# Performance work log

Hardware: AMD Instinct MI355X
Metric: run time of the kernel (lower is better)

Reference implementation:

```python
import jax, jax.numpy as jnp
import numpy as np

B, C, W, H = 2, 64, 96, 96  # N = W*H = 9216 spatial positions


def conv1x1(x, w, b):
    # x: (B, Cin, W, H), w: (Cout, Cin), b: (Cout,) -> (B, Cout, W, H)
    return jnp.einsum('bchw,oc->bohw', x, w) + b[None, :, None, None]


def setup_inputs() -> dict:
    key = jax.random.key(0)
    ks = jax.random.split(key, 4)
    c8 = C // 8
    s = 0.05  # small weight scale keeps softmax logits in a sane range
    return {
        'x': jax.random.normal(ks[0], (B, C, W, H), jnp.float32),
        'wq': jax.random.normal(ks[1], (c8, C), jnp.float32) * s,
        'bq': jnp.zeros((c8,), jnp.float32),
        'wk': jax.random.normal(ks[2], (c8, C), jnp.float32) * s,
        'bk': jnp.zeros((c8,), jnp.float32),
        'wv': jax.random.normal(ks[3], (C, C), jnp.float32) * s,
        'bv': jnp.zeros((C,), jnp.float32),
        'gamma': jnp.full((1,), 0.5, jnp.float32),
    }


def reference(x, wq, bq, wk, bk, wv, bv, gamma):
    b, c, w, h = x.shape
    n = w * h
    q = conv1x1(x, wq, bq).reshape(b, -1, n)   # (B, C//8, N)
    k = conv1x1(x, wk, bk).reshape(b, -1, n)   # (B, C//8, N)
    v = conv1x1(x, wv, bv).reshape(b, c, n)    # (B, C, N)
    energy = jnp.einsum('bci,bcj->bij', q, k)  # (B, N, N)
    attn = jax.nn.softmax(energy, axis=-1)
    # torch.bmm(v, attn): out[b,c,i] = sum_j v[b,c,j] * attn[b,j,i]
    out = jnp.einsum('bcj,bji->bci', v, attn).reshape(b, c, w, h)
    return gamma * out + x
```

## Files before the change

kernel.cpp:

```cpp
#include <hip/hip_runtime.h>

using half2v  = __attribute__((ext_vector_type(2))) _Float16;
using half4   = __attribute__((ext_vector_type(4))) _Float16;
using half8   = __attribute__((ext_vector_type(8))) _Float16;
using floatx4 = __attribute__((ext_vector_type(4))) float;

constexpr int BATCH = 2;
constexpr int NPOS  = 96 * 96;
constexpr int NT    = NPOS / 16;
constexpr int NST   = NPOS / 32;

#define EXP2(x) __builtin_amdgcn_exp2f(x)
#define MFMA16(A, B, C) __builtin_amdgcn_mfma_f32_16x16x16f16(A, B, C, 0, 0, 0)
#define MFMA32(A, B, C) __builtin_amdgcn_mfma_f32_16x16x32_f16(A, B, C, 0, 0, 0)

__device__ inline half8 p8_of(floatx4 e0, floatx4 e1) {
    half2v a0 = __builtin_bit_cast(half2v,
        __builtin_amdgcn_cvt_pkrtz(EXP2(e0[0]), EXP2(e0[1])));
    half2v a1 = __builtin_bit_cast(half2v,
        __builtin_amdgcn_cvt_pkrtz(EXP2(e0[2]), EXP2(e0[3])));
    half2v a2 = __builtin_bit_cast(half2v,
        __builtin_amdgcn_cvt_pkrtz(EXP2(e1[0]), EXP2(e1[1])));
    half2v a3 = __builtin_bit_cast(half2v,
        __builtin_amdgcn_cvt_pkrtz(EXP2(e1[2]), EXP2(e1[3])));
    half8 p = {a0[0], a0[1], a1[0], a1[1], a2[0], a2[1], a3[0], a3[1]};
    return p;
}

__global__ __launch_bounds__(256) void qkv_kernel(
    const float* __restrict__ x,
    const float* __restrict__ wq, const float* __restrict__ bq,
    const float* __restrict__ wk, const float* __restrict__ bk,
    const float* __restrict__ wv, const float* __restrict__ bv,
    _Float16* __restrict__ Qf, _Float16* __restrict__ Kf,
    _Float16* __restrict__ Vf)
{
    __shared__ float W[80][64];
    __shared__ float bias[80];
    __shared__ float qs[32][9];
    __shared__ float ks[32][9];
    __shared__ _Float16 vs[32][72];
    const int tid = threadIdx.x;
    for (int idx = tid; idx < 80 * 64; idx += 256) {
        int o = idx >> 6, c = idx & 63;
        float w;
        if (o < 8)       w = wq[o * 64 + c];
        else if (o < 16) w = wk[(o - 8) * 64 + c];
        else             w = wv[(o - 16) * 64 + c];
        W[o][c] = w;
    }
    if (tid < 80) {
        float bb;
        if (tid < 8)       bb = bq[tid];
        else if (tid < 16) bb = bk[tid - 8];
        else               bb = bv[tid - 16];
        bias[tid] = bb;
    }
    __syncthreads();

    const int js = blockIdx.x;
    const int b  = blockIdx.y;
    const int part = tid >> 5;
    const int jl   = tid & 31;
    const int i    = js * 32 + jl;

    float xr[64];
    #pragma unroll
    for (int c = 0; c < 64; ++c)
        xr[c] = x[(size_t)(b * 64 + c) * NPOS + i];

    #pragma unroll
    for (int q = 0; q < 10; ++q) {
        const int o = part * 10 + q;
        float s = bias[o];
        #pragma unroll
        for (int c4 = 0; c4 < 16; ++c4) {
            float4 w4 = *(const float4*)&W[o][c4 * 4];
            s += w4.x * xr[c4*4+0] + w4.y * xr[c4*4+1]
               + w4.z * xr[c4*4+2] + w4.w * xr[c4*4+3];
        }
        if (o < 8)       qs[jl][o] = s;
        else if (o < 16) ks[jl][o - 8] = s;
        else             vs[jl][o - 16] = (_Float16)s;
    }
    __syncthreads();

    const size_t tile = (size_t)b * NST + js;
    {
        const int ct = tid >> 6, l = tid & 63;
        const int g = l >> 4, cl = l & 15;
        half8 o8;
        #pragma unroll
        for (int idx = 0; idx < 8; ++idx)
            o8[idx] = vs[8 * g + idx][16 * ct + cl];
        *(half8*)&Vf[(tile * 256 + ct * 64 + l) * 8] = o8;
    }
    if (tid < 128) {
        const int l = tid >> 1, e = tid & 1;
        const int m = l & 15, g = l >> 4;
        const int jsrc = 8 * (m >> 2) + 4 * e + (m & 3);
        constexpr float LOG2E = 1.44269504088896f;
        half4 qh;
        #pragma unroll
        for (int r = 0; r < 4; ++r)
            qh[r] = (g < 2) ? (_Float16)(qs[jsrc][4 * g + r] * LOG2E)
                            : (_Float16)0.f;
        ((half4*)Qf)[(tile * 64 + l) * 2 + e] = qh;
    } else {
        const int t = tid - 128;
        const int ht = t >> 6, l = t & 63;
        const int il = l & 15, g = l >> 4;
        const int it = js * 2 + ht;
        half4 kh;
        #pragma unroll
        for (int r = 0; r < 4; ++r) {
            if (g < 2)       kh[r] = (_Float16)ks[16 * ht + il][4 * g + r];
            else if (g == 2) kh[r] = (r < 2) ? (_Float16)1.f : (_Float16)0.f;
            else             kh[r] = (_Float16)0.f;
        }
        ((half4*)Kf)[(size_t)(b * NT + it) * 64 + l] = kh;
    }
}

template<int JSPLIT>
__global__ __launch_bounds__(256, 3) void attn_kernel(
    const _Float16* __restrict__ Qf, const _Float16* __restrict__ Kf,
    const _Float16* __restrict__ Vf,
    float* __restrict__ part, float* __restrict__ part_rs)
{
    constexpr int NSTEP = NST / JSPLIT / 4;
    __shared__ half8 Pb[2][4][4][64];
    __shared__ float rsred[4][4][16];
    const int s   = blockIdx.x;
    const int jh  = blockIdx.y;
    const int b   = s & 1;
    const int igl = s >> 1;
    const int tid = threadIdx.x;
    const int w = tid >> 6, l = tid & 63;
    const int it0 = igl * 4, i0 = igl * 64;

    const half8* __restrict__ qfb = (const half8*)Qf + (size_t)b * NST * 64;
    const half4* __restrict__ kfb = (const half4*)Kf + (size_t)b * NT * 64;
    const half8* __restrict__ vfb = (const half8*)Vf + (size_t)b * NST * 256;

    half4 kf[4];
    #pragma unroll
    for (int st = 0; st < 4; ++st) kf[st] = kfb[(size_t)(it0 + st) * 64 + l];

    half8 vones;
    #pragma unroll
    for (int e = 0; e < 8; ++e)
        vones[e] = (_Float16)(((l & 15) == 0) ? 1.f : 0.f);

    floatx4 acc[4];
    floatx4 rs[4];
    #pragma unroll
    for (int st = 0; st < 4; ++st) {
        acc[st] = (floatx4){0.f, 0.f, 0.f, 0.f};
        rs[st]  = (floatx4){0.f, 0.f, 0.f, 0.f};
    }

    const floatx4 z = {0.f, 0.f, 0.f, 0.f};
    const int st0 = jh * (NST / JSPLIT);

    half8 qv = qfb[(size_t)(st0 + w) * 64 + l];

    for (int k = 0; k < NSTEP; ++k) {
        const int t4 = st0 + k * 4;
        const int buf = k & 1;
        half8 v0 = vfb[(size_t)(t4 + 0) * 256 + w * 64 + l];
        half8 v1 = vfb[(size_t)(t4 + 1) * 256 + w * 64 + l];
        half8 v2 = vfb[(size_t)(t4 + 2) * 256 + w * 64 + l];
        half8 v3 = vfb[(size_t)(t4 + 3) * 256 + w * 64 + l];

        {
            half4 qe0 = __builtin_shufflevector(qv, qv, 0, 1, 2, 3);
            half4 qe1 = __builtin_shufflevector(qv, qv, 4, 5, 6, 7);
            #pragma unroll
            for (int st = 0; st < 4; ++st) {
                floatx4 e0 = MFMA16(qe0, kf[st], z);
                floatx4 e1 = MFMA16(qe1, kf[st], z);
                half8 p = p8_of(e0, e1);
                rs[st] = MFMA32(vones, p, rs[st]);
                Pb[buf][w][st][l] = p;
            }
        }
        if (k + 1 < NSTEP)
            qv = qfb[(size_t)(st0 + (k + 1) * 4 + w) * 64 + l];

        __syncthreads();

        #pragma unroll
        for (int st = 0; st < 4; ++st) {
            acc[st] = MFMA32(v0, Pb[buf][0][st][l], acc[st]);
            acc[st] = MFMA32(v1, Pb[buf][1][st][l], acc[st]);
            acc[st] = MFMA32(v2, Pb[buf][2][st][l], acc[st]);
            acc[st] = MFMA32(v3, Pb[buf][3][st][l], acc[st]);
        }
    }

    float* __restrict__ P  = part    + (size_t)jh * ((size_t)BATCH * 64 * NPOS);
    float* __restrict__ Pr = part_rs + (size_t)jh * ((size_t)BATCH * NPOS);
    {
        const int iq = i0 + (l & 15);
        #pragma unroll
        for (int st = 0; st < 4; ++st)
            #pragma unroll
            for (int r = 0; r < 4; ++r) {
                int c = 16 * w + 4 * (l >> 4) + r;
                size_t o = ((size_t)(b * 64 + c)) * NPOS + iq + 16 * st;
                P[o] = acc[st][r];
            }
    }

    if (l < 16) {
        #pragma unroll
        for (int st = 0; st < 4; ++st) rsred[w][st][l] = rs[st][0];
    }
    __syncthreads();
    if (w == 0 && l < 16) {
        #pragma unroll
        for (int st = 0; st < 4; ++st) {
            float rsv = rsred[0][st][l] + rsred[1][st][l]
                      + rsred[2][st][l] + rsred[3][st][l];
            Pr[(size_t)b * NPOS + i0 + 16 * st + l] = rsv;
        }
    }
}

template<int JSPLIT>
__global__ __launch_bounds__(256) void combine_kernel(
    const float* __restrict__ part, const float* __restrict__ part_rs,
    const float* __restrict__ x, const float* __restrict__ gamma,
    float* __restrict__ out)
{
    const float g = gamma[0];
    const size_t idx = (size_t)blockIdx.x * 256 + threadIdx.x;
    const size_t stride  = ((size_t)BATCH * 64 * NPOS) / 4;
    const size_t rstride = ((size_t)BATCH * NPOS) / 4;
    const int i4 = (int)(idx % (NPOS / 4));
    const int b  = (int)(idx / ((size_t)64 * (NPOS / 4)));
    const float4* p0 = (const float4*)part;
    const float4* r0 = (const float4*)part_rs;

    float4 a = p0[idx];
    float4 rsum = r0[(size_t)b * (NPOS / 4) + i4];
    #pragma unroll
    for (int u = 1; u < JSPLIT; ++u) {
        float4 q = p0[idx + (size_t)u * stride];
        a.x += q.x; a.y += q.y; a.z += q.z; a.w += q.w;
        float4 rq = r0[(size_t)b * (NPOS / 4) + i4 + (size_t)u * rstride];
        rsum.x += rq.x; rsum.y += rq.y; rsum.z += rq.z; rsum.w += rq.w;
    }
    float4 xv = ((const float4*)x)[idx];
    float4 o;
    o.x = g * (a.x / rsum.x) + xv.x;
    o.y = g * (a.y / rsum.y) + xv.y;
    o.z = g * (a.z / rsum.z) + xv.z;
    o.w = g * (a.w / rsum.w) + xv.w;
    ((float4*)out)[idx] = o;
}

extern "C" void kernel_launch(void* const* d_in, const int* in_sizes, int n_in,
                              void* d_out, int out_size, void* d_ws, size_t ws_size,
                              hipStream_t stream)
{
    const float* x     = (const float*)d_in[0];
    const float* wq    = (const float*)d_in[1];
    const float* bq    = (const float*)d_in[2];
    const float* wk    = (const float*)d_in[3];
    const float* bk    = (const float*)d_in[4];
    const float* wv    = (const float*)d_in[5];
    const float* bv    = (const float*)d_in[6];
    const float* gamma = (const float*)d_in[7];
    float* out = (float*)d_out;

    char* wsb = (char*)d_ws;
    _Float16* Qf = (_Float16*)wsb;
    _Float16* Kf = (_Float16*)(wsb + 589824);
    _Float16* Vf = (_Float16*)(wsb + 1179648);
    float*    Pp = (float*)(wsb + 3538944);

    qkv_kernel<<<dim3(NST, BATCH), 256, 0, stream>>>(
        x, wq, bq, wk, bk, wv, bv, Qf, Kf, Vf);

    const size_t partBytes = (size_t)BATCH * 64 * NPOS * sizeof(float);
    const size_t rsBytes   = (size_t)BATCH * NPOS * sizeof(float);
    const size_t need4 = 3538944 + 4 * (partBytes + rsBytes);
    const int nblk = (BATCH * 64 * NPOS / 4) / 256;

    if (ws_size >= need4) {
        float* Prs = (float*)(wsb + 3538944 + 4 * partBytes);
        attn_kernel<4><<<dim3(NST, 4), 256, 0, stream>>>(Qf, Kf, Vf, Pp, Prs);
        combine_kernel<4><<<nblk, 256, 0, stream>>>(Pp, Prs, x, gamma, out);
    } else {
        float* Prs = (float*)(wsb + 3538944 + 2 * partBytes);
        attn_kernel<2><<<dim3(NST, 2), 256, 0, stream>>>(Qf, Kf, Vf, Pp, Prs);
        combine_kernel<2><<<nblk, 256, 0, stream>>>(Pp, Prs, x, gamma, out);
    }
}
```

Measured before the change: 123.8 us.

## Software-pipeline P production with PV accumulation across double-buffered LDS

Restructures the attention main loop so each iteration computes the next step's P tiles (QK MFMA plus exp) while consuming the previous step's P tiles from shared memory for the V·P accumulation. There is now one barrier per iteration instead of a produce/barrier/consume sequence. V and Q fragments are prefetched one step ahead into registers. The interleaving is meant to overlap exp/convert work with MFMA and hide global load latency, at the cost of more live registers and a prologue/epilogue.

```diff
diff --git a/kernel.cpp b/kernel.cpp
--- a/kernel.cpp
+++ b/kernel.cpp
@@ -163,41 +163,73 @@
     const floatx4 z = {0.f, 0.f, 0.f, 0.f};
     const int st0 = jh * (NST / JSPLIT);
 
+    #define PRODUCE(QV, BUF) do { \
+        half4 qe0 = __builtin_shufflevector(QV, QV, 0, 1, 2, 3); \
+        half4 qe1 = __builtin_shufflevector(QV, QV, 4, 5, 6, 7); \
+        _Pragma("unroll") \
+        for (int st = 0; st < 4; ++st) { \
+            floatx4 e0 = MFMA16(qe0, kf[st], z); \
+            floatx4 e1 = MFMA16(qe1, kf[st], z); \
+            half8 pw = p8_of(e0, e1); \
+            rs[st] = MFMA32(vones, pw, rs[st]); \
+            Pb[BUF][w][st][l] = pw; \
+        } \
+    } while (0)
+
     half8 qv = qfb[(size_t)(st0 + w) * 64 + l];
-
-    for (int k = 0; k < NSTEP; ++k) {
-        const int t4 = st0 + k * 4;
-        const int buf = k & 1;
-        half8 v0 = vfb[(size_t)(t4 + 0) * 256 + w * 64 + l];
-        half8 v1 = vfb[(size_t)(t4 + 1) * 256 + w * 64 + l];
-        half8 v2 = vfb[(size_t)(t4 + 2) * 256 + w * 64 + l];
-        half8 v3 = vfb[(size_t)(t4 + 3) * 256 + w * 64 + l];
+    half8 v0 = vfb[(size_t)(st0 + 0) * 256 + w * 64 + l];
+    half8 v1 = vfb[(size_t)(st0 + 1) * 256 + w * 64 + l];
+    half8 v2 = vfb[(size_t)(st0 + 2) * 256 + w * 64 + l];
+    half8 v3 = vfb[(size_t)(st0 + 3) * 256 + w * 64 + l];
+    PRODUCE(qv, 0);
+    qv = qfb[(size_t)(st0 + 4 + w) * 64 + l];
+    __syncthreads();
+
+    for (int k = 0; k < NSTEP - 1; ++k) {
+        const int b0 = k & 1, b1 = b0 ^ 1;
+        const int t4n = st0 + (k + 1) * 4;
+        half8 v0n = vfb[(size_t)(t4n + 0) * 256 + w * 64 + l];
+        half8 v1n = vfb[(size_t)(t4n + 1) * 256 + w * 64 + l];
+        half8 v2n = vfb[(size_t)(t4n + 2) * 256 + w * 64 + l];
+        half8 v3n = vfb[(size_t)(t4n + 3) * 256 + w * 64 + l];
+        const int kq = (k + 2 < NSTEP) ? (k + 2) : (NSTEP - 1);
+        half8 qn = qfb[(size_t)(st0 + kq * 4 + w) * 64 + l];
 
         {
             half4 qe0 = __builtin_shufflevector(qv, qv, 0, 1, 2, 3);
             half4 qe1 = __builtin_shufflevector(qv, qv, 4, 5, 6, 7);
             #pragma unroll
             for (int st = 0; st < 4; ++st) {
+                half8 p0 = Pb[b0][0][st][l];
+                half8 p1 = Pb[b0][1][st][l];
+                half8 p2 = Pb[b0][2][st][l];
+                half8 p3 = Pb[b0][3][st][l];
                 floatx4 e0 = MFMA16(qe0, kf[st], z);
                 floatx4 e1 = MFMA16(qe1, kf[st], z);
-                half8 p = p8_of(e0, e1);
-                rs[st] = MFMA32(vones, p, rs[st]);
-                Pb[buf][w][st][l] = p;
+                half8 pw = p8_of(e0, e1);
+                rs[st] = MFMA32(vones, pw, rs[st]);
+                Pb[b1][w][st][l] = pw;
+                acc[st] = MFMA32(v0, p0, acc[st]);
+                acc[st] = MFMA32(v1, p1, acc[st]);
+                acc[st] = MFMA32(v2, p2, acc[st]);
+                acc[st] = MFMA32(v3, p3, acc[st]);
             }
         }
-        if (k + 1 < NSTEP)
-            qv = qfb[(size_t)(st0 + (k + 1) * 4 + w) * 64 + l];
-
+        v0 = v0n; v1 = v1n; v2 = v2n; v3 = v3n; qv = qn;
         __syncthreads();
-
+    }
+
+    {
+        const int b0 = (NSTEP - 1) & 1;
         #pragma unroll
         for (int st = 0; st < 4; ++st) {
-            acc[st] = MFMA32(v0, Pb[buf][0][st][l], acc[st]);
-            acc[st] = MFMA32(v1, Pb[buf][1][st][l], acc[st]);
-            acc[st] = MFMA32(v2, Pb[buf][2][st][l], acc[st]);
-            acc[st] = MFMA32(v3, Pb[buf][3][st][l], acc[st]);
-        }
-    }
+            acc[st] = MFMA32(v0, Pb[b0][0][st][l], acc[st]);
+            acc[st] = MFMA32(v1, Pb[b0][1][st][l], acc[st]);
+            acc[st] = MFMA32(v2, Pb[b0][2][st][l], acc[st]);
+            acc[st] = MFMA32(v3, Pb[b0][3][st][l], acc[st]);
+        }
+    }
+    #undef PRODUCE
 
     float* __restrict__ P  = part    + (size_t)jh * ((size_t)BATCH * 64 * NPOS);
     float* __restrict__ Pr = part_rs + (size_t)jh * ((size_t)BATCH * NPOS);
```

New measurement: 122.7 us. About the same (-0.9%).

## Software-pipeline attention P tiles and split PV work across wave pairs

Applied to the files above, without the earlier changes.

Restructures the attention loop so each wave keeps its own P tile in registers. It reads only its partner wave's tile from shared memory, and the QK/exp stage of the next step overlaps the PV MFMAs of the previous step, with one barrier per step. Waves are paired by channel half and j-half. Each accumulates two 16-channel tiles over its own and its partner's P, and the two j-halves are merged through shared memory at the end. This doubles the accumulator registers and lowers launch_bounds occupancy from 3 to 2 blocks per CU.

```diff
diff --git a/kernel.cpp b/kernel.cpp
--- a/kernel.cpp
+++ b/kernel.cpp
@@ -123,13 +123,14 @@
 }
 
 template<int JSPLIT>
-__global__ __launch_bounds__(256, 3) void attn_kernel(
+__global__ __launch_bounds__(256, 2) void attn_kernel(
     const _Float16* __restrict__ Qf, const _Float16* __restrict__ Kf,
     const _Float16* __restrict__ Vf,
     float* __restrict__ part, float* __restrict__ part_rs)
 {
     constexpr int NSTEP = NST / JSPLIT / 4;
-    __shared__ half8 Pb[2][4][4][64];
+    __shared__ half8 P0[4][4][64];
+    __shared__ half8 P1[4][4][64];
     __shared__ float rsred[4][4][16];
     const int s   = blockIdx.x;
     const int jh  = blockIdx.y;
@@ -137,6 +138,7 @@
     const int igl = s >> 1;
     const int tid = threadIdx.x;
     const int w = tid >> 6, l = tid & 63;
+    const int wc = w & 1, wj = w >> 1;
     const int it0 = igl * 4, i0 = igl * 64;
 
     const half8* __restrict__ qfb = (const half8*)Qf + (size_t)b * NST * 64;
@@ -152,78 +154,144 @@
     for (int e = 0; e < 8; ++e)
         vones[e] = (_Float16)(((l & 15) == 0) ? 1.f : 0.f);
 
-    floatx4 acc[4];
+    floatx4 acc[4][2];
     floatx4 rs[4];
     #pragma unroll
     for (int st = 0; st < 4; ++st) {
-        acc[st] = (floatx4){0.f, 0.f, 0.f, 0.f};
-        rs[st]  = (floatx4){0.f, 0.f, 0.f, 0.f};
+        acc[st][0] = (floatx4){0.f, 0.f, 0.f, 0.f};
+        acc[st][1] = (floatx4){0.f, 0.f, 0.f, 0.f};
+        rs[st]     = (floatx4){0.f, 0.f, 0.f, 0.f};
     }
 
     const floatx4 z = {0.f, 0.f, 0.f, 0.f};
     const int st0 = jh * (NST / JSPLIT);
 
-    half8 qv = qfb[(size_t)(st0 + w) * 64 + l];
-
-    for (int k = 0; k < NSTEP; ++k) {
-        const int t4 = st0 + k * 4;
-        const int buf = k & 1;
-        half8 v0 = vfb[(size_t)(t4 + 0) * 256 + w * 64 + l];
-        half8 v1 = vfb[(size_t)(t4 + 1) * 256 + w * 64 + l];
-        half8 v2 = vfb[(size_t)(t4 + 2) * 256 + w * 64 + l];
-        half8 v3 = vfb[(size_t)(t4 + 3) * 256 + w * 64 + l];
-
-        {
-            half4 qe0 = __builtin_shufflevector(qv, qv, 0, 1, 2, 3);
-            half4 qe1 = __builtin_shufflevector(qv, qv, 4, 5, 6, 7);
+    const half8* qp = qfb + (size_t)(st0 + 8 + w) * 64 + l;
+    const half8* vb = vfb + (size_t)(st0 + 2 * wj) * 256 + wc * 128 + l;
+    const int o_own  = wc * 256;
+    const int o_part = 256 - o_own;
+
+    half8 qA = qfb[(size_t)(st0 + w) * 64 + l];
+    half8 qB = qfb[(size_t)(st0 + 4 + w) * 64 + l];
+    half8 pwA[4], pwB[4];
+
+    {
+        half4 qe0 = __builtin_shufflevector(qA, qA, 0, 1, 2, 3);
+        half4 qe1 = __builtin_shufflevector(qA, qA, 4, 5, 6, 7);
+        #pragma unroll
+        for (int ist = 0; ist < 4; ++ist) {
+            floatx4 e0 = MFMA16(qe0, kf[ist], z);
+            floatx4 e1 = MFMA16(qe1, kf[ist], z);
+            half8 pw = p8_of(e0, e1);
+            rs[ist] = MFMA32(vones, pw, rs[ist]);
+            P0[w][ist][l] = pw;
+            pwA[ist] = pw;
+        }
+    }
+    __syncthreads();
+
+    #define BODY(PRD, PWR, PWOLD, PWNEW, QUSE, QPRE) do { \
+        half8 pr0 = PRD[w ^ 1][0][l], pr1 = PRD[w ^ 1][1][l]; \
+        half8 pr2 = PRD[w ^ 1][2][l], pr3 = PRD[w ^ 1][3][l]; \
+        half8 vo0 = vb[o_own],  vo1 = vb[o_own + 64]; \
+        half8 vq0 = vb[o_part], vq1 = vb[o_part + 64]; \
+        QPRE = qp[0]; qp += 256; \
+        half4 qe0 = __builtin_shufflevector(QUSE, QUSE, 0, 1, 2, 3); \
+        half4 qe1 = __builtin_shufflevector(QUSE, QUSE, 4, 5, 6, 7); \
+        _Pragma("unroll") \
+        for (int ist = 0; ist < 4; ++ist) { \
+            floatx4 e0 = MFMA16(qe0, kf[ist], z); \
+            floatx4 e1 = MFMA16(qe1, kf[ist], z); \
+            half8 pw = p8_of(e0, e1); \
+            rs[ist] = MFMA32(vones, pw, rs[ist]); \
+            PWR[w][ist][l] = pw; \
+            PWNEW[ist] = pw; \
+        } \
+        _Pragma("unroll") \
+        for (int ist = 0; ist < 4; ++ist) { \
+            acc[ist][0] = MFMA32(vo0, PWOLD[ist], acc[ist][0]); \
+            acc[ist][1] = MFMA32(vo1, PWOLD[ist], acc[ist][1]); \
+        } \
+        acc[0][0] = MFMA32(vq0, pr0, acc[0][0]); \
+        acc[0][1] = MFMA32(vq1, pr0, acc[0][1]); \
+        acc[1][0] = MFMA32(vq0, pr1, acc[1][0]); \
+        acc[1][1] = MFMA32(vq1, pr1, acc[1][1]); \
+        acc[2][0] = MFMA32(vq0, pr2, acc[2][0]); \
+        acc[2][1] = MFMA32(vq1, pr2, acc[2][1]); \
+        acc[3][0] = MFMA32(vq0, pr3, acc[3][0]); \
+        acc[3][1] = MFMA32(vq1, pr3, acc[3][1]); \
+        vb += 1024; \
+        __syncthreads(); \
+    } while (0)
+
+    for (int t = 0; t < (NSTEP - 2) / 2; ++t) {
+        BODY(P0, P1, pwA, pwB, qB, qA);
+        BODY(P1, P0, pwB, pwA, qA, qB);
+    }
+    BODY(P0, P1, pwA, pwB, qB, qA);
+    #undef BODY
+
+    {
+        half8 pr0 = P1[w ^ 1][0][l], pr1 = P1[w ^ 1][1][l];
+        half8 pr2 = P1[w ^ 1][2][l], pr3 = P1[w ^ 1][3][l];
+        half8 vo0 = vb[o_own],  vo1 = vb[o_own + 64];
+        half8 vq0 = vb[o_part], vq1 = vb[o_part + 64];
+        #pragma unroll
+        for (int ist = 0; ist < 4; ++ist) {
+            acc[ist][0] = MFMA32(vo0, pwB[ist], acc[ist][0]);
+            acc[ist][1] = MFMA32(vo1, pwB[ist], acc[ist][1]);
+        }
+        acc[0][0] = MFMA32(vq0, pr0, acc[0][0]);
+        acc[0][1] = MFMA32(vq1, pr0, acc[0][1]);
+        acc[1][0] = MFMA32(vq0, pr1, acc[1][0]);
+        acc[1][1] = MFMA32(vq1, pr1, acc[1][1]);
+        acc[2][0] = MFMA32(vq0, pr2, acc[2][0]);
+        acc[2][1] = MFMA32(vq1, pr2, acc[2][1]);
+        acc[3][0] = MFMA32(vq0, pr3, acc[3][0]);
+        acc[3][1] = MFMA32(vq1, pr3, acc[3][1]);
+    }
+    __syncthreads();
+
+    float4* mrg = (float4*)&P0[0][0][0];
+    if (wj == 1) {
+        #pragma unroll
+        for (int ist = 0; ist < 4; ++ist)
             #pragma unroll
-            for (int st = 0; st < 4; ++st) {
-                floatx4 e0 = MFMA16(qe0, kf[st], z);
-                floatx4 e1 = MFMA16(qe1, kf[st], z);
-                half8 p = p8_of(e0, e1);
-                rs[st] = MFMA32(vones, p, rs[st]);
-                Pb[buf][w][st][l] = p;
-            }
-        }
-        if (k + 1 < NSTEP)
-            qv = qfb[(size_t)(st0 + (k + 1) * 4 + w) * 64 + l];
-
-        __syncthreads();
-
-        #pragma unroll
-        for (int st = 0; st < 4; ++st) {
-            acc[st] = MFMA32(v0, Pb[buf][0][st][l], acc[st]);
-            acc[st] = MFMA32(v1, Pb[buf][1][st][l], acc[st]);
-            acc[st] = MFMA32(v2, Pb[buf][2][st][l], acc[st]);
-            acc[st] = MFMA32(v3, Pb[buf][3][st][l], acc[st]);
-        }
-    }
+            for (int cti = 0; cti < 2; ++cti)
+                mrg[(size_t)((wc * 8 + ist * 2 + cti) * 64) + l] =
+                    *(float4*)&acc[ist][cti];
+    }
+    if (l < 16) {
+        #pragma unroll
+        for (int ist = 0; ist < 4; ++ist) rsred[w][ist][l] = rs[ist][0];
+    }
+    __syncthreads();
 
     float* __restrict__ P  = part    + (size_t)jh * ((size_t)BATCH * 64 * NPOS);
     float* __restrict__ Pr = part_rs + (size_t)jh * ((size_t)BATCH * NPOS);
-    {
+    if (wj == 0) {
         const int iq = i0 + (l & 15);
         #pragma unroll
-        for (int st = 0; st < 4; ++st)
+        for (int ist = 0; ist < 4; ++ist)
             #pragma unroll
-            for (int r = 0; r < 4; ++r) {
-                int c = 16 * w + 4 * (l >> 4) + r;
-                size_t o = ((size_t)(b * 64 + c)) * NPOS + iq + 16 * st;
-                P[o] = acc[st][r];
+            for (int cti = 0; cti < 2; ++cti) {
+                float4 m = mrg[(size_t)((wc * 8 + ist * 2 + cti) * 64) + l];
+                float4 a = *(float4*)&acc[ist][cti];
+                a.x += m.x; a.y += m.y; a.z += m.z; a.w += m.w;
+                #pragma unroll
+                for (int r = 0; r < 4; ++r) {
+                    int c = 16 * (2 * wc + cti) + 4 * (l >> 4) + r;
+                    size_t o = ((size_t)(b * 64 + c)) * NPOS + iq + 16 * ist;
+                    P[o] = (&a.x)[r];
+                }
             }
     }
-
-    if (l < 16) {
-        #pragma unroll
-        for (int st = 0; st < 4; ++st) rsred[w][st][l] = rs[st][0];
-    }
-    __syncthreads();
     if (w == 0 && l < 16) {
         #pragma unroll
-        for (int st = 0; st < 4; ++st) {
-            float rsv = rsred[0][st][l] + rsred[1][st][l]
-                      + rsred[2][st][l] + rsred[3][st][l];
-            Pr[(size_t)b * NPOS + i0 + 16 * st + l] = rsv;
+        for (int ist = 0; ist < 4; ++ist) {
+            float rsv = rsred[0][ist][l] + rsred[1][ist][l]
+                      + rsred[2][ist][l] + rsred[3][ist][l];
+            Pr[(size_t)b * NPOS + i0 + 16 * ist + l] = rsv;
         }
     }
 }
```

Result: no change. 123.6 us (-0.2%).
